# Optimization experiments

Hardware: AMD Instinct MI355X
Metric: run time of the kernel (lower is better)

The kernel has to match this reference:

```python
import jax, jax.numpy as jnp
import numpy as np

B, T, C, H = 8, 2048, 768, 768

def setup_inputs() -> dict:
    key = jax.random.key(0)
    ks = jax.random.split(key, 7)
    s = 1.0 / np.sqrt(C)
    return {
        "visual_token": jax.random.normal(ks[0], (B, T, C), dtype=jnp.float32),
        "Wk": jax.random.normal(ks[1], (H, C), dtype=jnp.float32) * s,
        "bk": jax.random.normal(ks[2], (H,), dtype=jnp.float32) * s,
        "Wq": jax.random.normal(ks[3], (H, C), dtype=jnp.float32) * s,
        "bq": jax.random.normal(ks[4], (H,), dtype=jnp.float32) * s,
        "W1": jax.random.normal(ks[5], (C, C), dtype=jnp.float32) * s,
        "W2": jax.random.normal(ks[6], (C, C), dtype=jnp.float32) * s,
    }

def reference(visual_token, Wk, bk, Wq, bq, W1, W2):
    x = visual_token
    k = jnp.einsum('btc,hc->bth', x, Wk) + bk          # [B,T,H]
    q = jnp.einsum('btc,hc->bth', x, Wq) + bq          # [B,T,H]
    scores = jnp.einsum('bih,bjh->bij', k, q)          # K @ Q^T, unscaled
    attn = jax.nn.softmax(scores, axis=1)              # NOTE: softmax over dim=1 as in source
    p = x + jnp.einsum('bij,bjc->bic', attn, x)        # residual with value = input
    h = jnp.einsum('btc,dc->btd', p, W1)               # f_1 (no bias)
    h = jnp.einsum('btd,ed->bte', h, W2)               # f_2 (no bias)
    return p + jax.nn.relu(h)
```

## Files before the change

kernel.cpp:

```cpp
#include <hip/hip_runtime.h>

typedef float    f32x4 __attribute__((ext_vector_type(4)));
typedef _Float16 f16x8 __attribute__((ext_vector_type(8)));

__device__ __forceinline__ void gload16(const void* g, void* l) {
  __builtin_amdgcn_global_load_lds(
      (__attribute__((address_space(1))) void*)(const void*)g,
      (__attribute__((address_space(3))) void*)l,
      16, 0, 0);
}

template <int EPI>
__global__ __launch_bounds__(512, 4) void gemm_kt(
    const _Float16* __restrict__ A, size_t sA, int lda,
    const _Float16* __restrict__ B, size_t sB, int ldb,
    float* __restrict__ out0, _Float16* __restrict__ out1,
    float* __restrict__ out2,
    size_t sO, int ldo,
    const float* __restrict__ bias,
    const float* __restrict__ resid,
    const _Float16* __restrict__ cf,
    int K) {
  __shared__ _Float16 lds[3 * 12288];
  __shared__ _Float16 clds[(EPI == 6) ? 4096 : 1];

  const int gx = gridDim.x, gy = gridDim.y;
  const int nblk = gx * gy * gridDim.z;
  int lin = (blockIdx.z * gy + blockIdx.y) * gx + blockIdx.x;
  lin = (lin & 7) * (nblk >> 3) + (lin >> 3);
  const int b  = lin / (gx * gy);
  const int r2 = lin - b * gx * gy;
  const int m0 = (r2 / gx) * 128;
  const int n0 = (r2 - (r2 / gx) * gx) * 256;

  const int t = threadIdx.x, lane = t & 63, w = t >> 6;
  const int wr = w >> 2;
  const int wc = w & 3;
  const int lr = lane & 15, lq = lane >> 4;

  const _Float16* Ab = A + (size_t)b * sA;
  const _Float16* Bb = B + (size_t)b * sB;

  const int arow = t >> 2;
  const int acol = ((t & 3) ^ ((arow >> 1) & 3)) * 8;
  const _Float16* a_src  = Ab + (size_t)(m0 + arow) * lda + acol;
  const _Float16* b_src0 = Bb + (size_t)(n0 + arow) * ldb + acol;
  const _Float16* b_src1 = b_src0 + (size_t)128 * ldb;
  const int a_dst  = t * 8;
  const int b_dst0 = 4096 + t * 8;
  const int b_dst1 = 4096 + (t + 512) * 8;

  const int swz  = ((lr >> 1) & 3) << 3;
  const int koff = (lq * 8) ^ swz;
  const int a_rd = (wr * 64 + lr) * 32 + koff;
  const int b_rd = 4096 + (wc * 64 + lr) * 32 + koff;

  f32x4 acc[4][4];
#pragma unroll
  for (int f = 0; f < 4; ++f)
#pragma unroll
    for (int j = 0; j < 4; ++j) acc[f][j] = (f32x4){0.f, 0.f, 0.f, 0.f};

  const int NT = K >> 5;

  if constexpr (EPI == 6)
    gload16(cf + ((size_t)b * 32 + (m0 >> 6)) * 2048 + t * 8, clds + t * 8);
  gload16(a_src,       lds + a_dst);
  gload16(b_src0,      lds + b_dst0);
  gload16(b_src1,      lds + b_dst1);
  gload16(a_src  + 32, lds + 12288 + a_dst);
  gload16(b_src0 + 32, lds + 12288 + b_dst0);
  gload16(b_src1 + 32, lds + 12288 + b_dst1);

  int buf = 0;
  for (int kt = 0; kt < NT; ++kt) {
    if (kt + 1 < NT) asm volatile("s_waitcnt vmcnt(3)" ::: "memory");
    else             asm volatile("s_waitcnt vmcnt(0)" ::: "memory");
    __builtin_amdgcn_s_barrier();
    __builtin_amdgcn_sched_barrier(0);

    const _Float16* lb = lds + buf * 12288;
    const int nb = (buf + 2 >= 3) ? buf - 1 : buf + 2;
    _Float16* ln = lds + nb * 12288;

    f16x8 af[4], bf[4], cv;
    if constexpr (EPI == 6)
      cv = *(const f16x8*)(clds + wr * 2048 + kt * 32 + lq * 8);
#pragma unroll
    for (int f = 0; f < 4; ++f) {
      af[f] = *(const f16x8*)(lb + a_rd + f * 512);
      if constexpr (EPI == 6) af[f] = af[f] * cv;
    }
#pragma unroll
    for (int j = 0; j < 4; ++j) bf[j] = *(const f16x8*)(lb + b_rd + j * 512);
    if (kt + 2 < NT) {
      const int ko = (kt + 2) * 32;
      gload16(a_src  + ko, ln + a_dst);
      gload16(b_src0 + ko, ln + b_dst0);
      gload16(b_src1 + ko, ln + b_dst1);
    }
    __builtin_amdgcn_s_setprio(1);
#pragma unroll
    for (int f = 0; f < 4; ++f)
#pragma unroll
      for (int j = 0; j < 4; ++j)
        acc[f][j] = __builtin_amdgcn_mfma_f32_16x16x32_f16(af[f], bf[j], acc[f][j], 0, 0, 0);
    __builtin_amdgcn_s_setprio(0);
    __builtin_amdgcn_sched_barrier(0);
    buf = (buf + 1 >= 3) ? 0 : buf + 1;
  }

  if constexpr (EPI == 4) {
#pragma unroll
    for (int j = 0; j < 4; ++j) {
      float m = -3.4e38f;
#pragma unroll
      for (int f = 0; f < 4; ++f)
#pragma unroll
        for (int r = 0; r < 4; ++r) m = fmaxf(m, acc[f][j][r]);
#pragma unroll
      for (int d = 16; d <= 32; d <<= 1) m = fmaxf(m, __shfl_xor(m, d, 64));
      float Z = 0.f;
      const int col = n0 + wc * 64 + j * 16 + lr;
#pragma unroll
      for (int f = 0; f < 4; ++f)
#pragma unroll
        for (int r = 0; r < 4; ++r) {
          const _Float16 eh = (_Float16)__expf(acc[f][j][r] - m);
          const int row = m0 + wr * 64 + f * 16 + lq * 4 + r;
          out1[(size_t)b * sO + (size_t)row * ldo + col] = eh;
          Z += (float)eh;
        }
#pragma unroll
      for (int d = 16; d <= 32; d <<= 1) Z += __shfl_xor(Z, d, 64);
      if (lq == 0) {
        const int chunk = (m0 >> 6) + wr;
        const size_t sidx = ((size_t)b * 32 + chunk) * 2048 + col;
        out0[sidx] = m;
        out2[sidx] = Z;
      }
    }
  } else {
#pragma unroll
    for (int f = 0; f < 4; ++f)
#pragma unroll
      for (int j = 0; j < 4; ++j)
#pragma unroll
        for (int r = 0; r < 4; ++r) {
          const int row = m0 + wr * 64 + f * 16 + lq * 4 + r;
          const int col = n0 + wc * 64 + j * 16 + lr;
          const size_t oidx = (size_t)b * sO + (size_t)row * ldo + col;
          float v = acc[f][j][r];
          if constexpr (EPI == 0) {
            if (bias) v += bias[col];
            out1[oidx] = (_Float16)v;
          } else if constexpr (EPI == 6) {
            const float pv = v + resid[oidx];
            out0[oidx] = pv;
            out1[oidx] = (_Float16)pv;
          } else {
            out0[oidx] = resid[oidx] + (v > 0.f ? v : 0.f);
          }
        }
  }
}

__global__ __launch_bounds__(256) void convert_f32_f16(const float* __restrict__ in,
                                                       _Float16* __restrict__ out, long n8) {
  long i = (long)blockIdx.x * blockDim.x + threadIdx.x;
  if (i >= n8) return;
  f32x4 v0 = *(const f32x4*)(in + i * 8);
  f32x4 v1 = *(const f32x4*)(in + i * 8 + 4);
  f16x8 o;
  o[0] = (_Float16)v0[0]; o[1] = (_Float16)v0[1]; o[2] = (_Float16)v0[2]; o[3] = (_Float16)v0[3];
  o[4] = (_Float16)v1[0]; o[5] = (_Float16)v1[1]; o[6] = (_Float16)v1[2]; o[7] = (_Float16)v1[3];
  *(f16x8*)(out + i * 8) = o;
}

__global__ void concat_bias(const float* __restrict__ bk, const float* __restrict__ bq,
                            float* __restrict__ bkq) {
  const int i = blockIdx.x * 256 + threadIdx.x;
  if (i < 768) bkq[i] = bk[i];
  else if (i < 1536) bkq[i] = bq[i - 768];
}

__global__ __launch_bounds__(256) void col_final(const float* __restrict__ pm,
                                                 const float* __restrict__ pZ,
                                                 _Float16* __restrict__ c) {
  const int b = blockIdx.z;
  const int col = blockIdx.x * 256 + threadIdx.x;
  float mv[32];
  float m = -3.4e38f;
#pragma unroll
  for (int k = 0; k < 32; ++k) {
    mv[k] = pm[((size_t)b * 32 + k) * 2048 + col];
    m = fmaxf(m, mv[k]);
  }
  float Z = 0.f;
#pragma unroll
  for (int k = 0; k < 32; ++k)
    Z += pZ[((size_t)b * 32 + k) * 2048 + col] * __expf(mv[k] - m);
  const float rZ = 1.f / Z;
#pragma unroll
  for (int k = 0; k < 32; ++k)
    c[((size_t)b * 32 + k) * 2048 + col] = (_Float16)(__expf(mv[k] - m) * rZ);
}

__global__ void transpose_f32_to_f16(const float* __restrict__ x, _Float16* __restrict__ xT) {
  __shared__ float tile[32][33];
  const int b = blockIdx.z;
  const int c0 = blockIdx.x * 32, j0 = blockIdx.y * 32;
  const float* xb  = x  + (size_t)b * 2048 * 768;
  _Float16*    xTb = xT + (size_t)b * 768 * 2048;
  const int tx = threadIdx.x, ty = threadIdx.y;
#pragma unroll
  for (int dy = 0; dy < 32; dy += 8)
    tile[ty + dy][tx] = xb[(size_t)(j0 + ty + dy) * 768 + c0 + tx];
  __syncthreads();
#pragma unroll
  for (int dy = 0; dy < 32; dy += 8)
    xTb[(size_t)(c0 + ty + dy) * 2048 + j0 + tx] = (_Float16)tile[tx][ty + dy];
}

extern "C" void kernel_launch(void* const* d_in, const int* in_sizes, int n_in,
                              void* d_out, int out_size, void* d_ws, size_t ws_size,
                              hipStream_t stream) {
  const float* x  = (const float*)d_in[0];
  const float* Wk = (const float*)d_in[1];
  const float* bk = (const float*)d_in[2];
  const float* Wq = (const float*)d_in[3];
  const float* bq = (const float*)d_in[4];
  const float* W1 = (const float*)d_in[5];
  const float* W2 = (const float*)d_in[6];
  float* out = (float*)d_out;

  char* ws = (char*)d_ws;
  size_t off = 0;
  auto alloc = [&](size_t bytes) -> char* {
    char* p = ws + off;
    off += (bytes + 255) & ~(size_t)255;
    return p;
  };
  _Float16* xf = (_Float16*)alloc(25165824);
  _Float16* kq = (_Float16*)alloc(50331648);
  _Float16* Wf = (_Float16*)alloc(4718592);
  _Float16* E  = (_Float16*)alloc(67108864);
  float*    pf32 = (float*)alloc(50331648);
  float*    pm = (float*)alloc(2097152);
  float*    pZ = (float*)alloc(2097152);
  float*    bkq  = (float*)alloc(6144);

  _Float16* Wkqf = Wf;
  _Float16* W1f  = Wf + 2 * 589824;
  _Float16* W2f  = Wf + 3 * 589824;
  _Float16* xT   = xf;
  _Float16* pf16 = kq;
  _Float16* cT   = kq + 12582912;
  _Float16* hf16 = kq + 12582912;

  const size_t sKQ = (size_t)2048 * 1536;
  const size_t sS  = (size_t)2048 * 2048;
  const size_t sKV = (size_t)2048 * 768;

  convert_f32_f16<<<6144, 256, 0, stream>>>(x,  xf, 1572864);
  convert_f32_f16<<<288,  256, 0, stream>>>(Wk, Wkqf, 73728);
  convert_f32_f16<<<288,  256, 0, stream>>>(Wq, Wkqf + 589824, 73728);
  convert_f32_f16<<<288,  256, 0, stream>>>(W1, W1f, 73728);
  convert_f32_f16<<<288,  256, 0, stream>>>(W2, W2f, 73728);
  concat_bias<<<6, 256, 0, stream>>>(bk, bq, bkq);

  gemm_kt<0><<<dim3(6, 128, 1), 512, 0, stream>>>(xf, 0, 768, Wkqf, 0, 768,
                                                  nullptr, kq, nullptr, 0, 1536,
                                                  bkq, nullptr, nullptr, 768);

  transpose_f32_to_f16<<<dim3(24, 64, 8), dim3(32, 8), 0, stream>>>(x, xT);

  gemm_kt<4><<<dim3(8, 16, 8), 512, 0, stream>>>(kq, sKQ, 1536, kq + 768, sKQ, 1536,
                                                 pm, E, pZ, sS, 2048,
                                                 nullptr, nullptr, nullptr, 768);
  col_final<<<dim3(8, 1, 8), 256, 0, stream>>>(pm, pZ, cT);

  gemm_kt<6><<<dim3(3, 16, 8), 512, 0, stream>>>(E, sS, 2048, xT, sKV, 2048,
                                                 pf32, pf16, nullptr, sKV, 768,
                                                 nullptr, x, cT, 2048);

  gemm_kt<0><<<dim3(3, 128, 1), 512, 0, stream>>>(pf16, 0, 768, W1f, 0, 768,
                                                  nullptr, hf16, nullptr, 0, 768,
                                                  nullptr, nullptr, nullptr, 768);

  gemm_kt<3><<<dim3(3, 128, 1), 512, 0, stream>>>(hf16, 0, 768, W2f, 0, 768,
                                                  out, nullptr, nullptr, 0, 768,
                                                  nullptr, pf32, nullptr, 768);
}
```

Baseline: 306.0 us.

## Fuse x conversion into transpose and drop fp32 residual buffer

Folds the f32-to-f16 conversion of x into the transpose kernel, so x is read once and both the row-major and transposed f16 copies are written from the same tile. The attention epilogue no longer writes an fp32 copy of p; the final GEMM reads the f16 p as its residual. This removes one full read of x and a large fp32 write and read, at the cost of rounding the residual to fp16 precision in the output.

```diff
diff --git a/kernel.cpp b/kernel.cpp
--- a/kernel.cpp
+++ b/kernel.cpp
@@ -2,6 +2,7 @@
 
 typedef float    f32x4 __attribute__((ext_vector_type(4)));
 typedef _Float16 f16x8 __attribute__((ext_vector_type(8)));
+typedef _Float16 f16x4 __attribute__((ext_vector_type(4)));
 
 __device__ __forceinline__ void gload16(const void* g, void* l) {
   __builtin_amdgcn_global_load_lds(
@@ -19,6 +20,7 @@
     size_t sO, int ldo,
     const float* __restrict__ bias,
     const float* __restrict__ resid,
+    const _Float16* __restrict__ residh,
     const _Float16* __restrict__ cf,
     int K) {
   __shared__ _Float16 lds[3 * 12288];
@@ -155,11 +157,9 @@
             if (bias) v += bias[col];
             out1[oidx] = (_Float16)v;
           } else if constexpr (EPI == 6) {
-            const float pv = v + resid[oidx];
-            out0[oidx] = pv;
-            out1[oidx] = (_Float16)pv;
+            out1[oidx] = (_Float16)(v + resid[oidx]);
           } else {
-            out0[oidx] = resid[oidx] + (v > 0.f ? v : 0.f);
+            out0[oidx] = (float)residh[oidx] + (v > 0.f ? v : 0.f);
           }
         }
   }
@@ -206,17 +206,26 @@
     c[((size_t)b * 32 + k) * 2048 + col] = (_Float16)(__expf(mv[k] - m) * rZ);
 }
 
-__global__ void transpose_f32_to_f16(const float* __restrict__ x, _Float16* __restrict__ xT) {
+__global__ void xprep(const float* __restrict__ x, _Float16* __restrict__ xf,
+                      _Float16* __restrict__ xT) {
   __shared__ float tile[32][33];
   const int b = blockIdx.z;
   const int c0 = blockIdx.x * 32, j0 = blockIdx.y * 32;
-  const float* xb  = x  + (size_t)b * 2048 * 768;
-  _Float16*    xTb = xT + (size_t)b * 768 * 2048;
+  const float* xb = x + (size_t)b * 2048 * 768;
   const int tx = threadIdx.x, ty = threadIdx.y;
 #pragma unroll
   for (int dy = 0; dy < 32; dy += 8)
     tile[ty + dy][tx] = xb[(size_t)(j0 + ty + dy) * 768 + c0 + tx];
   __syncthreads();
+  {
+    const int u = ty * 32 + tx;
+    const int row = u >> 3, c4 = (u & 7) * 4;
+    f16x4 o;
+#pragma unroll
+    for (int q = 0; q < 4; ++q) o[q] = (_Float16)tile[row][c4 + q];
+    *(f16x4*)(xf + ((size_t)b * 2048 + j0 + row) * 768 + c0 + c4) = o;
+  }
+  _Float16* xTb = xT + (size_t)b * 768 * 2048;
 #pragma unroll
   for (int dy = 0; dy < 32; dy += 8)
     xTb[(size_t)(c0 + ty + dy) * 2048 + j0 + tx] = (_Float16)tile[tx][ty + dy];
@@ -245,7 +254,7 @@
   _Float16* kq = (_Float16*)alloc(50331648);
   _Float16* Wf = (_Float16*)alloc(4718592);
   _Float16* E  = (_Float16*)alloc(67108864);
-  float*    pf32 = (float*)alloc(50331648);
+  _Float16* xT = (_Float16*)alloc(25165824);
   float*    pm = (float*)alloc(2097152);
   float*    pZ = (float*)alloc(2097152);
   float*    bkq  = (float*)alloc(6144);
@@ -253,7 +262,6 @@
   _Float16* Wkqf = Wf;
   _Float16* W1f  = Wf + 2 * 589824;
   _Float16* W2f  = Wf + 3 * 589824;
-  _Float16* xT   = xf;
   _Float16* pf16 = kq;
   _Float16* cT   = kq + 12582912;
   _Float16* hf16 = kq + 12582912;
@@ -262,33 +270,31 @@
   const size_t sS  = (size_t)2048 * 2048;
   const size_t sKV = (size_t)2048 * 768;
 
-  convert_f32_f16<<<6144, 256, 0, stream>>>(x,  xf, 1572864);
-  convert_f32_f16<<<288,  256, 0, stream>>>(Wk, Wkqf, 73728);
-  convert_f32_f16<<<288,  256, 0, stream>>>(Wq, Wkqf + 589824, 73728);
-  convert_f32_f16<<<288,  256, 0, stream>>>(W1, W1f, 73728);
-  convert_f32_f16<<<288,  256, 0, stream>>>(W2, W2f, 73728);
+  xprep<<<dim3(24, 64, 8), dim3(32, 8), 0, stream>>>(x, xf, xT);
+  convert_f32_f16<<<288, 256, 0, stream>>>(Wk, Wkqf, 73728);
+  convert_f32_f16<<<288, 256, 0, stream>>>(Wq, Wkqf + 589824, 73728);
+  convert_f32_f16<<<288, 256, 0, stream>>>(W1, W1f, 73728);
+  convert_f32_f16<<<288, 256, 0, stream>>>(W2, W2f, 73728);
   concat_bias<<<6, 256, 0, stream>>>(bk, bq, bkq);
 
   gemm_kt<0><<<dim3(6, 128, 1), 512, 0, stream>>>(xf, 0, 768, Wkqf, 0, 768,
                                                   nullptr, kq, nullptr, 0, 1536,
-                                                  bkq, nullptr, nullptr, 768);
-
-  transpose_f32_to_f16<<<dim3(24, 64, 8), dim3(32, 8), 0, stream>>>(x, xT);
+                                                  bkq, nullptr, nullptr, nullptr, 768);
 
   gemm_kt<4><<<dim3(8, 16, 8), 512, 0, stream>>>(kq, sKQ, 1536, kq + 768, sKQ, 1536,
                                                  pm, E, pZ, sS, 2048,
-                                                 nullptr, nullptr, nullptr, 768);
+                                                 nullptr, nullptr, nullptr, nullptr, 768);
   col_final<<<dim3(8, 1, 8), 256, 0, stream>>>(pm, pZ, cT);
 
   gemm_kt<6><<<dim3(3, 16, 8), 512, 0, stream>>>(E, sS, 2048, xT, sKV, 2048,
-                                                 pf32, pf16, nullptr, sKV, 768,
-                                                 nullptr, x, cT, 2048);
+                                                 nullptr, pf16, nullptr, sKV, 768,
+                                                 nullptr, x, nullptr, cT, 2048);
 
   gemm_kt<0><<<dim3(3, 128, 1), 512, 0, stream>>>(pf16, 0, 768, W1f, 0, 768,
                                                   nullptr, hf16, nullptr, 0, 768,
-                                                  nullptr, nullptr, nullptr, 768);
+                                                  nullptr, nullptr, nullptr, nullptr, 768);
 
   gemm_kt<3><<<dim3(3, 128, 1), 512, 0, stream>>>(hf16, 0, 768, W2f, 0, 768,
                                                   out, nullptr, nullptr, 0, 768,
-                                                  nullptr, pf32, nullptr, 768);
-}
+                                                  nullptr, nullptr, pf16, nullptr, 768);
+}
```

New measurement: 282.9 us. 1.08x faster.
